# Kernel tuning notes

Measured on AMD Instinct MI355X. Metric: run time of the kernel, lower is better.

## Reference

```python
import jax, jax.numpy as jnp
import numpy as np

B, S_PREV, E, H, LOW = 8, 4095, 2048, 16, 512
HD = E // H  # 128
ROPE_BASE = 10000.0


def _rope(x, pos):
    # x: [..., S, d], pos: [S]; half-split rotary
    d = x.shape[-1]
    half = d // 2
    inv_freq = 1.0 / (ROPE_BASE ** (jnp.arange(half, dtype=jnp.float32) / half))
    ang = pos.astype(jnp.float32)[:, None] * inv_freq  # [S, half]
    cos, sin = jnp.cos(ang), jnp.sin(ang)
    x1, x2 = x[..., :half], x[..., half:]
    return jnp.concatenate([x1 * cos - x2 * sin, x1 * sin + x2 * cos], axis=-1)


def setup_inputs() -> dict:
    key = jax.random.key(0)
    ks = jax.random.split(key, 10)

    def w(k, *shape):
        return jax.random.normal(k, shape, dtype=jnp.float32) * (1.0 / np.float32(np.sqrt(shape[0])))

    return {
        "x": jax.random.normal(ks[0], (B, 1, E), dtype=jnp.float32),
        "ckv_cache": jax.random.normal(ks[1], (B, S_PREV, LOW), dtype=jnp.float32),
        "kr_cache": jax.random.normal(ks[2], (B, S_PREV, HD), dtype=jnp.float32),
        "Wdq": w(ks[3], E, E),
        "Wuq": w(ks[4], E, E),
        "Wqr": w(ks[5], E, HD),
        "Wdkv": w(ks[6], E, LOW),
        "Wkr": w(ks[7], E, HD),
        "fused_upsample": w(ks[8], LOW, 2 * E),
        "Wo": w(ks[9], E, E),
    }


def reference(x, ckv_cache, kr_cache, Wdq, Wuq, Wqr, Wdkv, Wkr, fused_upsample, Wo):
    Bx = x.shape[0]
    # update compressed KV caches with the current token
    ckv = jnp.concatenate([ckv_cache, x @ Wdkv], axis=1)            # [B,S,LOW]
    kr = jnp.concatenate([kr_cache, x @ Wkr], axis=1)               # [B,S,HD]
    S = ckv.shape[1]
    up = ckv @ fused_upsample                                       # [B,S,2E]
    k_up, v = up[..., :E], up[..., E:]
    Kc = k_up.reshape(Bx, S, H, HD).transpose(0, 2, 1, 3)           # [B,H,S,HD]
    Kr = _rope(kr, jnp.arange(S))                                   # [B,S,HD] shared rope-K
    Kr = jnp.broadcast_to(Kr[:, None], (Bx, H, S, HD))
    v = v.reshape(Bx, S, H, HD).transpose(0, 2, 1, 3)               # [B,H,S,HD]
    # query path
    Cq = x @ Wdq                                                    # [B,1,E]
    Qc = (Cq @ Wuq).reshape(Bx, 1, H, HD).transpose(0, 2, 1, 3)     # [B,H,1,HD]
    Qr = _rope(Cq @ Wqr, jnp.arange(S - 1, S))                      # [B,1,HD] at last pos
    Qr = jnp.broadcast_to(Qr[:, None], (Bx, H, 1, HD))
    q = jnp.concatenate([Qc, Qr], axis=-1)                          # [B,H,1,2HD]
    k = jnp.concatenate([Kc, Kr], axis=-1)                          # [B,H,S,2HD]
    scores = jnp.einsum('bhqd,bhkd->bhqk', q, k) / np.float32(np.sqrt(2 * HD))
    attn = jax.nn.softmax(scores, axis=-1)
    o = jnp.einsum('bhqk,bhkd->bhqd', attn, v)                      # [B,H,1,HD]
    out = o.transpose(0, 2, 1, 3).reshape(Bx, 1, E) @ Wo            # [B,1,E]
    return out
```

## Files before the change

### kernel.cpp

```cpp
#include <hip/hip_runtime.h>
#include <hip/hip_bf16.h>

#define B_ 8
#define SPREV 4095
#define S_ 4096
#define E_ 2048
#define H_ 16
#define HD_ 128
#define LOW_ 512
#define NCH 64
#define CHK 64
#define L2INV 0.207620506f

typedef short s8v __attribute__((ext_vector_type(8)));
typedef float f4v __attribute__((ext_vector_type(4)));

__device__ __forceinline__ short f2bf_s(float f) {
  return (short)__bfloat16_as_ushort(__float2bfloat16(f));
}
__device__ __forceinline__ float bf2f(unsigned short h) {
  union { unsigned u; float f; } v; v.u = ((unsigned)h) << 16;
  return v.f;
}

__global__ __launch_bounds__(256) void init_kernel(float* __restrict__ ws_pre,
                                                   float* __restrict__ out) {
  int i = blockIdx.x * 256 + threadIdx.x;
  if (i < 55296) ws_pre[i] = 0.f;
  else if (i < 71680) out[i - 55296] = 0.f;
}

__global__ __launch_bounds__(128) void matvec8(
    const float* __restrict__ x, int K,
    const float* __restrict__ W0, int N0, float* __restrict__ o0,
    const float* __restrict__ W1, int N1, float* __restrict__ o1,
    const float* __restrict__ W2, int N2, float* __restrict__ o2)
{
  int cb = blockIdx.x;
  int nb0 = N0 >> 7, nb1 = N1 >> 7;
  const float* W; float* o; int N, colbase;
  if (cb < nb0)            { W = W0; o = o0; N = N0; colbase = cb << 7; }
  else if (cb < nb0 + nb1) { W = W1; o = o1; N = N1; colbase = (cb - nb0) << 7; }
  else                     { W = W2; o = o2; N = N2; colbase = (cb - nb0 - nb1) << 7; }
  int col = colbase + threadIdx.x;
  int k0 = blockIdx.y * 32;
  float acc[B_];
  #pragma unroll
  for (int b = 0; b < B_; ++b) acc[b] = 0.f;
  const float* Wp = W + (size_t)k0 * N + col;
  #pragma unroll 8
  for (int k = 0; k < 32; ++k) {
    float wv = Wp[(size_t)k * N];
    #pragma unroll
    for (int b = 0; b < B_; ++b)
      acc[b] = fmaf(x[b * K + k0 + k], wv, acc[b]);
  }
  #pragma unroll
  for (int b = 0; b < B_; ++b) atomicAdd(&o[b * N + col], acc[b]);
}

__global__ __launch_bounds__(256) void qeff_kernel(
    const float* __restrict__ Qc, const float* __restrict__ FU,
    unsigned short* __restrict__ qeff)
{
  int bx = blockIdx.x, b = blockIdx.y, t = threadIdx.x;
  int h = bx >> 2, lq = bx & 3;
  int g = t >> 4, li = t & 15;
  __shared__ float qs[HD_];
  if (t < 128) qs[t] = Qc[b * E_ + h * HD_ + t];
  __syncthreads();
  f4v q0 = *(const f4v*)&qs[li * 8];
  f4v q1 = *(const f4v*)&qs[li * 8 + 4];
  #pragma unroll 2
  for (int p = 0; p < 8; ++p) {
    int l = lq * 128 + p * 16 + g;
    const f4v* w4 = (const f4v*)(FU + (size_t)l * (2 * E_) + h * HD_ + li * 8);
    f4v w0 = w4[0], w1 = w4[1];
    float a = w0[0]*q0[0] + w0[1]*q0[1] + w0[2]*q0[2] + w0[3]*q0[3]
            + w1[0]*q1[0] + w1[1]*q1[1] + w1[2]*q1[2] + w1[3]*q1[3];
    a += __shfl_xor(a, 1); a += __shfl_xor(a, 2);
    a += __shfl_xor(a, 4); a += __shfl_xor(a, 8);
    if (li == 0) qeff[(size_t)(b * H_ + h) * LOW_ + l] = (unsigned short)f2bf_s(a);
  }
}

__global__ __launch_bounds__(512) void attn_kernel(
    const float* __restrict__ ckv_cache, const float* __restrict__ ckv_new,
    const unsigned short* __restrict__ qeff,
    const float* __restrict__ kr_cache, const float* __restrict__ kr_new,
    const float* __restrict__ qr_pre,
    unsigned short* __restrict__ acc_part, float* __restrict__ m_part,
    float* __restrict__ l_part)
{
  int chunk = blockIdx.x, b = blockIdx.y;
  int tid = threadIdx.x;
  int w = tid >> 6, lane = tid & 63;
  int kg = lane >> 4, l16 = lane & 15;
  __shared__ float S_lds[2][16 * 64];
  __shared__ unsigned short P_lds[16 * 64];
  __shared__ float qr_sh[128];
  __shared__ float rope_lds[64];

  if (tid < 64) {
    float invf = exp2f(-L2INV * (float)tid);
    float x1 = qr_pre[b * HD_ + tid], x2 = qr_pre[b * HD_ + 64 + tid];
    float sn, cs; sincosf(4095.0f * invf, &sn, &cs);
    qr_sh[tid]      = x1 * cs - x2 * sn;
    qr_sh[64 + tid] = x1 * sn + x2 * cs;
  }
  __syncthreads();

  {
    int kh = w >> 2;
    int s_loc = (w & 3) * 16 + l16;
    int s = chunk * CHK + s_loc;
    const float* crow = (s == S_ - 1) ? (ckv_new + b * LOW_)
                                      : (ckv_cache + ((size_t)b * SPREV + s) * LOW_);
    f4v acc0 = {0.f, 0.f, 0.f, 0.f};
    f4v acc1 = {0.f, 0.f, 0.f, 0.f};
    const s8v* qf = (const s8v*)(qeff + (size_t)(b * H_ + l16) * LOW_);
    #pragma unroll
    for (int kt = 0; kt < 4; ++kt) {
      #pragma unroll
      for (int half = 0; half < 2; ++half) {
        int kk = kh * 8 + kt * 2 + half;
        s8v a = qf[kk * 4 + kg];
        const float* cp = crow + kk * 32 + kg * 8;
        f4v c0 = *(const f4v*)cp;
        f4v c1 = *(const f4v*)(cp + 4);
        s8v bv;
        bv[0]=f2bf_s(c0[0]); bv[1]=f2bf_s(c0[1]); bv[2]=f2bf_s(c0[2]); bv[3]=f2bf_s(c0[3]);
        bv[4]=f2bf_s(c1[0]); bv[5]=f2bf_s(c1[1]); bv[6]=f2bf_s(c1[2]); bv[7]=f2bf_s(c1[3]);
        if (half == 0)
          acc0 = __builtin_amdgcn_mfma_f32_16x16x32_bf16(a, bv, acc0, 0, 0, 0);
        else
          acc1 = __builtin_amdgcn_mfma_f32_16x16x32_bf16(a, bv, acc1, 0, 0, 0);
      }
    }
    #pragma unroll
    for (int r = 0; r < 4; ++r) {
      int h = kg * 4 + r;
      S_lds[kh][h * 64 + (s_loc ^ ((h & 7) << 2))] = acc0[r] + acc1[r];
    }
    if (w < 4) {
      const float* krp = (s == S_ - 1) ? (kr_new + b * HD_)
                                       : (kr_cache + ((size_t)b * SPREV + s) * HD_);
      float fs = (float)s;
      float rdot = 0.f;
      #pragma unroll
      for (int q = 0; q < 4; ++q) {
        int j = kg * 16 + q * 4;
        f4v x1 = *(const f4v*)&krp[j];
        f4v x2 = *(const f4v*)&krp[64 + j];
        f4v qa = *(const f4v*)&qr_sh[j];
        f4v qb = *(const f4v*)&qr_sh[64 + j];
        #pragma unroll
        for (int k2 = 0; k2 < 4; ++k2) {
          float invf = exp2f(-L2INV * (float)(j + k2));
          float sn, cs; sincosf(fs * invf, &sn, &cs);
          rdot += qa[k2] * (x1[k2] * cs - x2[k2] * sn)
                + qb[k2] * (x1[k2] * sn + x2[k2] * cs);
        }
      }
      rdot += __shfl_xor(rdot, 16);
      rdot += __shfl_xor(rdot, 32);
      if (kg == 0) rope_lds[s_loc] = rdot;
    }
  }
  __syncthreads();

  {
    int half = lane >> 5;
    int h = w * 2 + half;
    int sl = lane & 31;
    int s0 = sl * 2;
    int c2 = (h & 7) << 2;
    float v0 = (S_lds[0][h * 64 + (s0 ^ c2)] + S_lds[1][h * 64 + (s0 ^ c2)]
                + rope_lds[s0]) * 0.0625f;
    float v1 = (S_lds[0][h * 64 + ((s0 + 1) ^ c2)] + S_lds[1][h * 64 + ((s0 + 1) ^ c2)]
                + rope_lds[s0 + 1]) * 0.0625f;
    float m = fmaxf(v0, v1);
    m = fmaxf(m, __shfl_xor(m, 1));  m = fmaxf(m, __shfl_xor(m, 2));
    m = fmaxf(m, __shfl_xor(m, 4));  m = fmaxf(m, __shfl_xor(m, 8));
    m = fmaxf(m, __shfl_xor(m, 16));
    float e0 = expf(v0 - m), e1 = expf(v1 - m);
    float lsum = e0 + e1;
    lsum += __shfl_xor(lsum, 1);  lsum += __shfl_xor(lsum, 2);
    lsum += __shfl_xor(lsum, 4);  lsum += __shfl_xor(lsum, 8);
    lsum += __shfl_xor(lsum, 16);
    unsigned pk = (unsigned)(unsigned short)f2bf_s(e0) |
                  ((unsigned)(unsigned short)f2bf_s(e1) << 16);
    *(unsigned*)&P_lds[h * 64 + (s0 ^ ((h & 7) << 3))] = pk;
    if (sl == 0) {
      int idx = (b * NCH + chunk) * H_ + h;
      m_part[idx] = m;
      l_part[idx] = lsum;
    }
  }
  __syncthreads();

  {
    s8v pa[2];
    const float* rp[2][8];
    #pragma unroll
    for (int kt = 0; kt < 2; ++kt) {
      int so = kt * 32 + kg * 8;
      pa[kt] = *(const s8v*)&P_lds[l16 * 64 + (so ^ ((l16 & 7) << 3))];
      #pragma unroll
      for (int i = 0; i < 8; ++i) {
        int s = chunk * CHK + so + i;
        rp[kt][i] = (s == S_ - 1) ? (ckv_new + b * LOW_)
                                  : (ckv_cache + ((size_t)b * SPREV + s) * LOW_);
      }
    }
    f4v oa[4];
    #pragma unroll
    for (int nt = 0; nt < 4; ++nt) oa[nt] = {0.f, 0.f, 0.f, 0.f};
    #pragma unroll
    for (int nt = 0; nt < 4; ++nt) {
      int l = w * 64 + nt * 16 + l16;
      #pragma unroll
      for (int kt = 0; kt < 2; ++kt) {
        s8v bv;
        #pragma unroll
        for (int i = 0; i < 8; ++i) bv[i] = (short)f2bf_s(rp[kt][i][l]);
        oa[nt] = __builtin_amdgcn_mfma_f32_16x16x32_bf16(pa[kt], bv, oa[nt], 0, 0, 0);
      }
    }
    size_t base = (size_t)(b * NCH + chunk) * H_;
    #pragma unroll
    for (int nt = 0; nt < 4; ++nt) {
      int l = w * 64 + nt * 16 + l16;
      #pragma unroll
      for (int r = 0; r < 4; ++r) {
        int h = kg * 4 + r;
        acc_part[(base + h) * LOW_ + l] = (unsigned short)f2bf_s(oa[nt][r]);
      }
    }
  }
}

__global__ __launch_bounds__(128) void reduce_proj_kernel(
    const float* __restrict__ m_part, const float* __restrict__ l_part,
    const unsigned short* __restrict__ acc_part, const float* __restrict__ FU,
    float* __restrict__ o_heads)
{
  int h = blockIdx.x, b = blockIdx.y, lz = blockIdx.z, t = threadIdx.x;
  __shared__ float wls[NCH];
  __shared__ float Linv_s;
  __shared__ float pa0[128], pa1[128];
  __shared__ float wl_sh[64];
  if (t < 64) {
    float mc = m_part[(b * NCH + t) * H_ + h];
    float M = mc;
    #pragma unroll
    for (int d = 1; d < 64; d <<= 1) M = fmaxf(M, __shfl_xor(M, d));
    float wc = expf(mc - M);
    float L = l_part[(b * NCH + t) * H_ + h] * wc;
    #pragma unroll
    for (int d = 1; d < 64; d <<= 1) L += __shfl_xor(L, d);
    wls[t] = wc;
    if (t == 0) Linv_s = 1.0f / L;
  }
  __syncthreads();
  {
    int p = t & 31, ch = t >> 5;
    int l0 = lz * 64 + p * 2;
    float a0 = 0.f, a1 = 0.f;
    const unsigned short* ap =
        acc_part + ((size_t)(b * NCH + ch * 16) * H_ + h) * LOW_ + l0;
    #pragma unroll 4
    for (int c = 0; c < 16; ++c) {
      unsigned pk = *(const unsigned*)(ap + (size_t)c * H_ * LOW_);
      float wc = wls[ch * 16 + c];
      a0 = fmaf(bf2f((unsigned short)(pk & 0xffffu)), wc, a0);
      a1 = fmaf(bf2f((unsigned short)(pk >> 16)),     wc, a1);
    }
    pa0[t] = a0; pa1[t] = a1;
  }
  __syncthreads();
  if (t < 32) {
    float inv = Linv_s;
    float s0 = pa0[t] + pa0[t + 32] + pa0[t + 64] + pa0[t + 96];
    float s1 = pa1[t] + pa1[t + 32] + pa1[t + 64] + pa1[t + 96];
    wl_sh[t * 2]     = s0 * inv;
    wl_sh[t * 2 + 1] = s1 * inv;
  }
  __syncthreads();
  {
    float a = 0.f;
    const float* fp = FU + (size_t)(lz * 64) * (2 * E_) + E_ + h * HD_ + t;
    #pragma unroll 4
    for (int l = 0; l < 64; ++l)
      a = fmaf(wl_sh[l], fp[(size_t)l * (2 * E_)], a);
    atomicAdd(&o_heads[(b * H_ + h) * HD_ + t], a);
  }
}

extern "C" void kernel_launch(void* const* d_in, const int* in_sizes, int n_in,
                              void* d_out, int out_size, void* d_ws, size_t ws_size,
                              hipStream_t stream)
{
  const float* x    = (const float*)d_in[0];
  const float* ckvc = (const float*)d_in[1];
  const float* krc  = (const float*)d_in[2];
  const float* Wdq  = (const float*)d_in[3];
  const float* Wuq  = (const float*)d_in[4];
  const float* Wqr  = (const float*)d_in[5];
  const float* Wdkv = (const float*)d_in[6];
  const float* Wkr  = (const float*)d_in[7];
  const float* FU   = (const float*)d_in[8];
  const float* Wo   = (const float*)d_in[9];
  float* out = (float*)d_out;

  char* ws = (char*)d_ws;
  float* Cq             = (float*)(ws + 0);
  float* Qc             = (float*)(ws + 65536);
  float* qr_pre         = (float*)(ws + 131072);
  float* ckvn           = (float*)(ws + 135168);
  float* krn            = (float*)(ws + 151552);
  float* o_heads        = (float*)(ws + 155648);
  unsigned short* qeff  = (unsigned short*)(ws + 221184);
  float* m_part         = (float*)(ws + 352256);
  float* l_part         = (float*)(ws + 385024);
  unsigned short* accp  = (unsigned short*)(ws + 417792);

  init_kernel<<<280, 256, 0, stream>>>((float*)ws, out);

  matvec8<<<dim3(21, 64), 128, 0, stream>>>(x, E_, Wdq, E_, Cq,
                                            Wdkv, LOW_, ckvn, Wkr, HD_, krn);
  matvec8<<<dim3(17, 64), 128, 0, stream>>>(Cq, E_, Wuq, E_, Qc,
                                            Wqr, HD_, qr_pre,
                                            (const float*)nullptr, 0, (float*)nullptr);
  qeff_kernel<<<dim3(64, 8), 256, 0, stream>>>(Qc, FU, qeff);
  attn_kernel<<<dim3(64, 8), 512, 0, stream>>>(ckvc, ckvn, qeff, krc, krn,
                                               qr_pre, accp, m_part, l_part);
  reduce_proj_kernel<<<dim3(16, 8, 8), 128, 0, stream>>>(m_part, l_part, accp,
                                                         FU, o_heads);
  matvec8<<<dim3(16, 64), 128, 0, stream>>>(o_heads, E_, Wo, E_, out,
                                            (const float*)nullptr, 0, (float*)nullptr,
                                            (const float*)nullptr, 0, (float*)nullptr);
}
```

Baseline: 83.11 us.

## Stage ckv chunk in LDS via direct global-to-LDS loads, halve chunk size

```diff
diff --git a/kernel.cpp b/kernel.cpp
--- a/kernel.cpp
+++ b/kernel.cpp
@@ -8,12 +8,15 @@
 #define H_ 16
 #define HD_ 128
 #define LOW_ 512
-#define NCH 64
-#define CHK 64
+#define NCH 128
+#define CHK 32
 #define L2INV 0.207620506f
 
 typedef short s8v __attribute__((ext_vector_type(8)));
 typedef float f4v __attribute__((ext_vector_type(4)));
+
+#define GAS(p) ((const __attribute__((address_space(1))) void*)(p))
+#define LAS(p) ((__attribute__((address_space(3))) void*)(p))
 
 __device__ __forceinline__ short f2bf_s(float f) {
   return (short)__bfloat16_as_ushort(__float2bfloat16(f));
@@ -96,10 +99,11 @@
   int tid = threadIdx.x;
   int w = tid >> 6, lane = tid & 63;
   int kg = lane >> 4, l16 = lane & 15;
-  __shared__ float S_lds[2][16 * 64];
-  __shared__ unsigned short P_lds[16 * 64];
+  __shared__ float V32[CHK * 512];
+  __shared__ float S_lds[4][16 * 32];
+  __shared__ unsigned short P_lds[16 * 32];
   __shared__ float qr_sh[128];
-  __shared__ float rope_lds[64];
+  __shared__ float rope_lds[CHK];
 
   if (tid < 64) {
     float invf = exp2f(-L2INV * (float)tid);
@@ -108,41 +112,53 @@
     qr_sh[tid]      = x1 * cs - x2 * sn;
     qr_sh[64 + tid] = x1 * sn + x2 * cs;
   }
-  __syncthreads();
-
-  {
-    int kh = w >> 2;
-    int s_loc = (w & 3) * 16 + l16;
-    int s = chunk * CHK + s_loc;
-    const float* crow = (s == S_ - 1) ? (ckv_new + b * LOW_)
-                                      : (ckv_cache + ((size_t)b * SPREV + s) * LOW_);
+
+  {
+    char* vbase = (char*)V32;
+    #pragma unroll
+    for (int i = 0; i < 8; ++i) {
+      int seg = w * 8 + i;
+      int r = seg >> 1, half = seg & 1;
+      int sg = chunk * CHK + r;
+      const float* crow = (sg == S_ - 1) ? (ckv_new + b * LOW_)
+                                         : (ckv_cache + ((size_t)b * SPREV + sg) * LOW_);
+      int c = (r & 7) ^ ((r >> 3) & 7);
+      const float* gp = crow + (((half * 64 + lane) ^ c) << 2);
+      __builtin_amdgcn_global_load_lds(GAS(gp), LAS(vbase + seg * 1024), 16, 0, 0);
+    }
+  }
+  __syncthreads();
+
+  {
+    int kq = w >> 1;
+    int s_loc = (w & 1) * 16 + l16;
+    int c = (s_loc & 7) ^ ((s_loc >> 3) & 7);
+    const float* vrow = V32 + s_loc * 512;
     f4v acc0 = {0.f, 0.f, 0.f, 0.f};
     f4v acc1 = {0.f, 0.f, 0.f, 0.f};
     const s8v* qf = (const s8v*)(qeff + (size_t)(b * H_ + l16) * LOW_);
     #pragma unroll
-    for (int kt = 0; kt < 4; ++kt) {
-      #pragma unroll
-      for (int half = 0; half < 2; ++half) {
-        int kk = kh * 8 + kt * 2 + half;
-        s8v a = qf[kk * 4 + kg];
-        const float* cp = crow + kk * 32 + kg * 8;
-        f4v c0 = *(const f4v*)cp;
-        f4v c1 = *(const f4v*)(cp + 4);
-        s8v bv;
-        bv[0]=f2bf_s(c0[0]); bv[1]=f2bf_s(c0[1]); bv[2]=f2bf_s(c0[2]); bv[3]=f2bf_s(c0[3]);
-        bv[4]=f2bf_s(c1[0]); bv[5]=f2bf_s(c1[1]); bv[6]=f2bf_s(c1[2]); bv[7]=f2bf_s(c1[3]);
-        if (half == 0)
-          acc0 = __builtin_amdgcn_mfma_f32_16x16x32_bf16(a, bv, acc0, 0, 0, 0);
-        else
-          acc1 = __builtin_amdgcn_mfma_f32_16x16x32_bf16(a, bv, acc1, 0, 0, 0);
-      }
+    for (int u = 0; u < 4; ++u) {
+      int kk = kq * 4 + u;
+      s8v a = qf[kk * 4 + kg];
+      int g = kk * 8 + kg * 2;
+      f4v c0 = *(const f4v*)(vrow + ((g ^ c) << 2));
+      f4v c1 = *(const f4v*)(vrow + (((g + 1) ^ c) << 2));
+      s8v bv;
+      bv[0]=f2bf_s(c0[0]); bv[1]=f2bf_s(c0[1]); bv[2]=f2bf_s(c0[2]); bv[3]=f2bf_s(c0[3]);
+      bv[4]=f2bf_s(c1[0]); bv[5]=f2bf_s(c1[1]); bv[6]=f2bf_s(c1[2]); bv[7]=f2bf_s(c1[3]);
+      if (u & 1)
+        acc1 = __builtin_amdgcn_mfma_f32_16x16x32_bf16(a, bv, acc1, 0, 0, 0);
+      else
+        acc0 = __builtin_amdgcn_mfma_f32_16x16x32_bf16(a, bv, acc0, 0, 0, 0);
     }
     #pragma unroll
     for (int r = 0; r < 4; ++r) {
       int h = kg * 4 + r;
-      S_lds[kh][h * 64 + (s_loc ^ ((h & 7) << 2))] = acc0[r] + acc1[r];
-    }
-    if (w < 4) {
+      S_lds[kq][h * 32 + (s_loc ^ ((h & 7) << 2))] = acc0[r] + acc1[r];
+    }
+    if (kq == 0) {
+      int s = chunk * CHK + s_loc;
       const float* krp = (s == S_ - 1) ? (kr_new + b * HD_)
                                        : (kr_cache + ((size_t)b * SPREV + s) * HD_);
       float fs = (float)s;
@@ -170,27 +186,21 @@
   __syncthreads();
 
   {
-    int half = lane >> 5;
-    int h = w * 2 + half;
-    int sl = lane & 31;
-    int s0 = sl * 2;
+    int h = tid >> 5, sl = tid & 31;
     int c2 = (h & 7) << 2;
-    float v0 = (S_lds[0][h * 64 + (s0 ^ c2)] + S_lds[1][h * 64 + (s0 ^ c2)]
-                + rope_lds[s0]) * 0.0625f;
-    float v1 = (S_lds[0][h * 64 + ((s0 + 1) ^ c2)] + S_lds[1][h * 64 + ((s0 + 1) ^ c2)]
-                + rope_lds[s0 + 1]) * 0.0625f;
-    float m = fmaxf(v0, v1);
+    float v = (S_lds[0][h * 32 + (sl ^ c2)] + S_lds[1][h * 32 + (sl ^ c2)]
+             + S_lds[2][h * 32 + (sl ^ c2)] + S_lds[3][h * 32 + (sl ^ c2)]
+             + rope_lds[sl]) * 0.0625f;
+    float m = v;
     m = fmaxf(m, __shfl_xor(m, 1));  m = fmaxf(m, __shfl_xor(m, 2));
     m = fmaxf(m, __shfl_xor(m, 4));  m = fmaxf(m, __shfl_xor(m, 8));
     m = fmaxf(m, __shfl_xor(m, 16));
-    float e0 = expf(v0 - m), e1 = expf(v1 - m);
-    float lsum = e0 + e1;
+    float e = expf(v - m);
+    float lsum = e;
     lsum += __shfl_xor(lsum, 1);  lsum += __shfl_xor(lsum, 2);
     lsum += __shfl_xor(lsum, 4);  lsum += __shfl_xor(lsum, 8);
     lsum += __shfl_xor(lsum, 16);
-    unsigned pk = (unsigned)(unsigned short)f2bf_s(e0) |
-                  ((unsigned)(unsigned short)f2bf_s(e1) << 16);
-    *(unsigned*)&P_lds[h * 64 + (s0 ^ ((h & 7) << 3))] = pk;
+    P_lds[h * 32 + (sl ^ ((h & 3) << 3))] = (unsigned short)f2bf_s(e);
     if (sl == 0) {
       int idx = (b * NCH + chunk) * H_ + h;
       m_part[idx] = m;
@@ -200,32 +210,22 @@
   __syncthreads();
 
   {
-    s8v pa[2];
-    const float* rp[2][8];
-    #pragma unroll
-    for (int kt = 0; kt < 2; ++kt) {
-      int so = kt * 32 + kg * 8;
-      pa[kt] = *(const s8v*)&P_lds[l16 * 64 + (so ^ ((l16 & 7) << 3))];
+    s8v pa = *(const s8v*)&P_lds[l16 * 32 + ((kg * 8) ^ ((l16 & 3) << 3))];
+    f4v oa[4];
+    #pragma unroll
+    for (int nt = 0; nt < 4; ++nt) oa[nt] = {0.f, 0.f, 0.f, 0.f};
+    #pragma unroll
+    for (int nt = 0; nt < 4; ++nt) {
+      int l = w * 64 + nt * 16 + l16;
+      int g = l >> 2, e = l & 3;
+      s8v bv;
       #pragma unroll
       for (int i = 0; i < 8; ++i) {
-        int s = chunk * CHK + so + i;
-        rp[kt][i] = (s == S_ - 1) ? (ckv_new + b * LOW_)
-                                  : (ckv_cache + ((size_t)b * SPREV + s) * LOW_);
+        int r = kg * 8 + i;
+        int c = (r & 7) ^ ((r >> 3) & 7);
+        bv[i] = f2bf_s(V32[r * 512 + ((g ^ c) << 2) + e]);
       }
-    }
-    f4v oa[4];
-    #pragma unroll
-    for (int nt = 0; nt < 4; ++nt) oa[nt] = {0.f, 0.f, 0.f, 0.f};
-    #pragma unroll
-    for (int nt = 0; nt < 4; ++nt) {
-      int l = w * 64 + nt * 16 + l16;
-      #pragma unroll
-      for (int kt = 0; kt < 2; ++kt) {
-        s8v bv;
-        #pragma unroll
-        for (int i = 0; i < 8; ++i) bv[i] = (short)f2bf_s(rp[kt][i][l]);
-        oa[nt] = __builtin_amdgcn_mfma_f32_16x16x32_bf16(pa[kt], bv, oa[nt], 0, 0, 0);
-      }
+      oa[nt] = __builtin_amdgcn_mfma_f32_16x16x32_bf16(pa, bv, oa[nt], 0, 0, 0);
     }
     size_t base = (size_t)(b * NCH + chunk) * H_;
     #pragma unroll
@@ -246,45 +246,47 @@
     float* __restrict__ o_heads)
 {
   int h = blockIdx.x, b = blockIdx.y, lz = blockIdx.z, t = threadIdx.x;
+  int w = t >> 6, lane = t & 63;
   __shared__ float wls[NCH];
-  __shared__ float Linv_s;
+  __shared__ float red[4];
   __shared__ float pa0[128], pa1[128];
   __shared__ float wl_sh[64];
-  if (t < 64) {
-    float mc = m_part[(b * NCH + t) * H_ + h];
-    float M = mc;
-    #pragma unroll
-    for (int d = 1; d < 64; d <<= 1) M = fmaxf(M, __shfl_xor(M, d));
-    float wc = expf(mc - M);
-    float L = l_part[(b * NCH + t) * H_ + h] * wc;
-    #pragma unroll
-    for (int d = 1; d < 64; d <<= 1) L += __shfl_xor(L, d);
-    wls[t] = wc;
-    if (t == 0) Linv_s = 1.0f / L;
-  }
-  __syncthreads();
+  float mc = m_part[(b * NCH + t) * H_ + h];
+  float M = mc;
+  #pragma unroll
+  for (int d = 1; d < 64; d <<= 1) M = fmaxf(M, __shfl_xor(M, d));
+  if (lane == 0) red[w] = M;
+  __syncthreads();
+  M = fmaxf(red[0], red[1]);
+  float wc = expf(mc - M);
+  wls[t] = wc;
+  float L = l_part[(b * NCH + t) * H_ + h] * wc;
+  #pragma unroll
+  for (int d = 1; d < 64; d <<= 1) L += __shfl_xor(L, d);
+  if (lane == 0) red[2 + w] = L;
+  __syncthreads();
+  float Linv = 1.0f / (red[2] + red[3]);
   {
     int p = t & 31, ch = t >> 5;
     int l0 = lz * 64 + p * 2;
     float a0 = 0.f, a1 = 0.f;
     const unsigned short* ap =
-        acc_part + ((size_t)(b * NCH + ch * 16) * H_ + h) * LOW_ + l0;
+        acc_part + ((size_t)(b * NCH + ch * 32) * H_ + h) * LOW_ + l0;
     #pragma unroll 4
-    for (int c = 0; c < 16; ++c) {
+    for (int c = 0; c < 32; ++c) {
       unsigned pk = *(const unsigned*)(ap + (size_t)c * H_ * LOW_);
-      float wc = wls[ch * 16 + c];
-      a0 = fmaf(bf2f((unsigned short)(pk & 0xffffu)), wc, a0);
-      a1 = fmaf(bf2f((unsigned short)(pk >> 16)),     wc, a1);
+      float wc2 = wls[ch * 32 + c];
+      a0 = fmaf(bf2f((unsigned short)(pk & 0xffffu)), wc2, a0);
+      a1 = fmaf(bf2f((unsigned short)(pk >> 16)),     wc2, a1);
     }
     pa0[t] = a0; pa1[t] = a1;
   }
   __syncthreads();
   if (t < 32) {
-    float inv = Linv_s;
     float s0 = pa0[t] + pa0[t + 32] + pa0[t + 64] + pa0[t + 96];
     float s1 = pa1[t] + pa1[t + 32] + pa1[t + 64] + pa1[t + 96];
-    wl_sh[t * 2]     = s0 * inv;
-    wl_sh[t * 2 + 1] = s1 * inv;
+    wl_sh[t * 2]     = s0 * Linv;
+    wl_sh[t * 2 + 1] = s1 * Linv;
   }
   __syncthreads();
   {
@@ -322,8 +324,8 @@
   float* o_heads        = (float*)(ws + 155648);
   unsigned short* qeff  = (unsigned short*)(ws + 221184);
   float* m_part         = (float*)(ws + 352256);
-  float* l_part         = (float*)(ws + 385024);
-  unsigned short* accp  = (unsigned short*)(ws + 417792);
+  float* l_part         = (float*)(ws + 417792);
+  unsigned short* accp  = (unsigned short*)(ws + 483328);
 
   init_kernel<<<280, 256, 0, stream>>>((float*)ws, out);
 
@@ -333,8 +335,8 @@
                                             Wqr, HD_, qr_pre,
                                             (const float*)nullptr, 0, (float*)nullptr);
   qeff_kernel<<<dim3(64, 8), 256, 0, stream>>>(Qc, FU, qeff);
-  attn_kernel<<<dim3(64, 8), 512, 0, stream>>>(ckvc, ckvn, qeff, krc, krn,
-                                               qr_pre, accp, m_part, l_part);
+  attn_kernel<<<dim3(128, 8), 512, 0, stream>>>(ckvc, ckvn, qeff, krc, krn,
+                                                qr_pre, accp, m_part, l_part);
   reduce_proj_kernel<<<dim3(16, 8, 8), 128, 0, stream>>>(m_part, l_part, accp,
                                                          FU, o_heads);
   matvec8<<<dim3(16, 64), 128, 0, stream>>>(o_heads, E_, Wo, E_, out,
```

New measurement: 92.21 us. 10.9% more time.
